# Optimization experiments

Measured on AMD Instinct MI355X. Metric: run time of the kernel, lower is better.

## Reference

```python
import jax, jax.numpy as jnp
import numpy as np

B, T, C = 4, 2048, 1024
H = 16
HD = C // H  # 64


def setup_inputs() -> dict:
    key = jax.random.key(0)
    k1, k2, k3 = jax.random.split(key, 3)
    x = jax.random.normal(k1, (B, T, C), dtype=jnp.float32)
    W_qkv = jax.random.normal(k2, (3 * C, C), dtype=jnp.float32) * (C ** -0.5)
    W_proj = jax.random.normal(k3, (C, C), dtype=jnp.float32) * (C ** -0.5)
    b_proj = jnp.zeros((C,), dtype=jnp.float32)
    return {"x": x, "W_qkv": W_qkv, "W_proj": W_proj, "b_proj": b_proj}


def reference(x, W_qkv, W_proj, b_proj):
    # qkv = x @ W_qkv.T : [B,T,3C]
    qkv = jnp.einsum('btc,oc->bto', x, W_qkv)
    # Faithful to torch: view(B,T,H,3*HD) then chunk last dim -> per-head q/k/v
    qkv = qkv.reshape(B, T, H, 3 * HD)
    q, k, v = jnp.split(qkv, 3, axis=-1)      # each [B,T,H,HD]
    q = q.transpose(0, 2, 1, 3)               # [B,H,T,HD]
    k = k.transpose(0, 2, 1, 3)
    v = v.transpose(0, 2, 1, 3)
    scale = HD ** -0.5
    att = jnp.einsum('bhqd,bhkd->bhqk', q, k) * scale  # [B,H,T,T]
    causal = jnp.tril(jnp.ones((T, T), dtype=bool))
    att = jnp.where(causal, att, -jnp.inf)
    att = jax.nn.softmax(att, axis=-1)
    out = jnp.einsum('bhqk,bhkd->bhqd', att, v)        # [B,H,T,HD]
    out = out.transpose(0, 2, 1, 3).reshape(B, T, C)
    out = jnp.einsum('btc,oc->bto', out, W_proj) + b_proj
    return out
```

## Files before the change

### kernel.cpp

```cpp
#include <hip/hip_runtime.h>
#include <stdint.h>

#define B_ 4
#define T_ 2048
#define C_ 1024
#define H_ 16
#define HD_ 64

typedef __attribute__((ext_vector_type(8))) short short8;
typedef __attribute__((ext_vector_type(4))) float f32x4;

typedef uint32_t __attribute__((address_space(3))) lds_u32;
typedef const uint32_t __attribute__((address_space(1))) glb_u32;

__device__ inline void async16(const void* g, void* l) {
    __builtin_amdgcn_global_load_lds((glb_u32*)g, (lds_u32*)l, 16, 0, 0);
}

__device__ inline short f2bf(float f) {
    union { float f; uint32_t u; } x; x.f = f;
    uint32_t r = (x.u + 0x7fffu + ((x.u >> 16) & 1u)) >> 16;
    return (short)r;
}
__device__ inline float bf2f(short b) {
    union { uint32_t u; float f; } x; x.u = ((uint32_t)(uint16_t)b) << 16;
    return x.f;
}

__global__ void detect_f32(const uint32_t* __restrict__ x, int* __restrict__ flag) {
    __shared__ int cnt;
    if (threadIdx.x == 0) cnt = 0;
    __syncthreads();
    int sane = 0;
    for (int i = threadIdx.x; i < 1024; i += 256) {
        float v = bf2f((short)(x[i] & 0xFFFFu));
        float a = fabsf(v);
        if (a > 1e-5f && a < 1e5f) sane++;
    }
    atomicAdd(&cnt, sane);
    __syncthreads();
    if (threadIdx.x == 0) *flag = (cnt < 512) ? 1 : 0;
}

__global__ void to_bf16(const void* __restrict__ src, short* __restrict__ dst,
                        int n, const int* __restrict__ flag) {
    const int i = (blockIdx.x * blockDim.x + threadIdx.x) * 8;
    if (i >= n) return;
    if (*flag) {
        const float* s = (const float*)src;
        short8 o;
#pragma unroll
        for (int j = 0; j < 8; j++) o[j] = f2bf(s[i + j]);
        *(short8*)&dst[i] = o;
    } else {
        *(short8*)&dst[i] = *(const short8*)((const short*)src + i);
    }
}

template <bool DUAL>
__global__ __launch_bounds__(256) void gemm_bt(
    const short* __restrict__ A, const short* __restrict__ Bm,
    const short* __restrict__ bias_bf, void* __restrict__ Cout,
    int M, int N, int K, const int* __restrict__ flag)
{
    __shared__ short As[128 * 32];
    __shared__ short Bs[128 * 32];
    const int tid  = threadIdx.x;
    const int lane = tid & 63;
    const int wave = tid >> 6;
    const int quad = lane >> 4;
    const int lcol = lane & 15;
    const int m0 = blockIdx.y * 128;
    const int n0 = blockIdx.x * 128;
    const int wm = (wave >> 1) * 64;
    const int wn = (wave & 1) * 64;
    const int isf32 = DUAL ? *flag : 0;

    f32x4 acc[4][4];
#pragma unroll
    for (int i = 0; i < 4; i++)
#pragma unroll
        for (int j = 0; j < 4; j++) acc[i][j] = f32x4{0.f, 0.f, 0.f, 0.f};

    const int idx0 = tid * 8;
    const int row0 = idx0 >> 5, col0 = idx0 & 31;
    const int idx1 = (256 + tid) * 8;
    const int row1 = idx1 >> 5, col1 = idx1 & 31;

    for (int k0 = 0; k0 < K; k0 += 32) {
        async16(&A[(size_t)(m0 + row0) * K + k0 + col0], &As[idx0]);
        async16(&A[(size_t)(m0 + row1) * K + k0 + col1], &As[idx1]);
        async16(&Bm[(size_t)(n0 + row0) * K + k0 + col0], &Bs[idx0]);
        async16(&Bm[(size_t)(n0 + row1) * K + k0 + col1], &Bs[idx1]);
        __syncthreads();

        short8 af[4], bfr[4];
#pragma unroll
        for (int mi = 0; mi < 4; mi++)
            af[mi] = *(const short8*)&As[(wm + mi * 16 + lcol) * 32 + quad * 8];
#pragma unroll
        for (int ni = 0; ni < 4; ni++)
            bfr[ni] = *(const short8*)&Bs[(wn + ni * 16 + lcol) * 32 + quad * 8];
#pragma unroll
        for (int mi = 0; mi < 4; mi++)
#pragma unroll
            for (int ni = 0; ni < 4; ni++)
                acc[mi][ni] = __builtin_amdgcn_mfma_f32_16x16x32_bf16(
                    af[mi], bfr[ni], acc[mi][ni], 0, 0, 0);
        __syncthreads();
    }

#pragma unroll
    for (int ni = 0; ni < 4; ni++) {
        const int col = n0 + wn + ni * 16 + lcol;
        const float bv = bias_bf ? bf2f(bias_bf[col]) : 0.f;
#pragma unroll
        for (int mi = 0; mi < 4; mi++) {
            const int row = m0 + wm + mi * 16 + quad * 4;
#pragma unroll
            for (int r = 0; r < 4; r++) {
                const float val = acc[mi][ni][r] + bv;
                const size_t off = (size_t)(row + r) * N + col;
                if (DUAL && isf32) ((float*)Cout)[off] = val;
                else               ((short*)Cout)[off] = f2bf(val);
            }
        }
    }
}

__global__ __launch_bounds__(256) void attn(const short* __restrict__ qkv,
                                            short* __restrict__ att)
{
    __shared__ short lds_k[64][72];
    __shared__ short lds_vt[64][68];
    __shared__ short lds_p[4][16][76];

    const int tid  = threadIdx.x;
    const int lane = tid & 63;
    const int wave = tid >> 6;
    const int quad = lane >> 4;
    const int lcol = lane & 15;

    const int j    = blockIdx.x & 7;
    const int bh   = blockIdx.x >> 3;
    const int b    = bh >> 4;
    const int h    = bh & 15;

    const size_t rowstride = 3 * C_;
    const size_t bhbase = (size_t)b * T_ * rowstride + (size_t)h * (3 * HD_);

    const int kkey = tid >> 2;
    const int kdp  = (tid & 3) * 16;
    const int vkey = tid & 63;
    const int vd0  = (tid >> 6) * 16;

    short8 kA, kB, vA, vB;
    auto load_tile = [&](int k0) {
        const size_t kb = bhbase + (size_t)(k0 + kkey) * rowstride + HD_ + kdp;
        kA = *(const short8*)&qkv[kb];
        kB = *(const short8*)&qkv[kb + 8];
        const size_t vb = bhbase + (size_t)(k0 + vkey) * rowstride + 2 * HD_ + vd0;
        vA = *(const short8*)&qkv[vb];
        vB = *(const short8*)&qkv[vb + 8];
    };

    const float LOG2E_SCALE = 0.1803368801f;

    auto process_chunk = [&](int qblk, bool sync_first) {
        const int q0 = qblk * 128;
        const int qA = q0 + wave * 16;
        const int qB = q0 + 64 + wave * 16;

        short8 qfA0, qfA1, qfB0, qfB1;
        {
            const size_t ba = bhbase + (size_t)(qA + lcol) * rowstride + quad * 8;
            qfA0 = *(const short8*)&qkv[ba];
            qfA1 = *(const short8*)&qkv[ba + 32];
            const size_t bb = bhbase + (size_t)(qB + lcol) * rowstride + quad * 8;
            qfB0 = *(const short8*)&qkv[bb];
            qfB1 = *(const short8*)&qkv[bb + 32];
        }

        f32x4 oA[4], oB[4];
#pragma unroll
        for (int i = 0; i < 4; i++) { oA[i] = f32x4{0.f,0.f,0.f,0.f}; oB[i] = f32x4{0.f,0.f,0.f,0.f}; }
        float lA[4] = {0.f,0.f,0.f,0.f}, lB[4] = {0.f,0.f,0.f,0.f};

        load_tile(0);

        const int LT = 2 * qblk + 1;
        for (int kt = 0; kt <= LT; ++kt) {
            if (kt || sync_first) __syncthreads();
            *(short8*)&lds_k[kkey][kdp]     = kA;
            *(short8*)&lds_k[kkey][kdp + 8] = kB;
#pragma unroll
            for (int jj = 0; jj < 8; jj++) {
                lds_vt[vd0 + jj][vkey]     = vA[jj];
                lds_vt[vd0 + 8 + jj][vkey] = vB[jj];
            }
            __syncthreads();
            if (kt < LT) load_tile((kt + 1) * 64);

            const int k0 = kt * 64;
            const bool doA = (kt < LT);

            f32x4 SA[4], SB[4];
#pragma unroll
            for (int t = 0; t < 4; t++) {
                const short8 kf0 = *(const short8*)&lds_k[t * 16 + lcol][quad * 8];
                const short8 kf1 = *(const short8*)&lds_k[t * 16 + lcol][32 + quad * 8];
                SB[t] = f32x4{0.f, 0.f, 0.f, 0.f};
                SB[t] = __builtin_amdgcn_mfma_f32_16x16x32_bf16(qfB0, kf0, SB[t], 0, 0, 0);
                SB[t] = __builtin_amdgcn_mfma_f32_16x16x32_bf16(qfB1, kf1, SB[t], 0, 0, 0);
                if (doA) {
                    SA[t] = f32x4{0.f, 0.f, 0.f, 0.f};
                    SA[t] = __builtin_amdgcn_mfma_f32_16x16x32_bf16(qfA0, kf0, SA[t], 0, 0, 0);
                    SA[t] = __builtin_amdgcn_mfma_f32_16x16x32_bf16(qfA1, kf1, SA[t], 0, 0, 0);
                }
            }

            short8 vf[4][2];
#pragma unroll
            for (int dt = 0; dt < 4; dt++) {
                vf[dt][0] = *(const short8*)&lds_vt[dt * 16 + lcol][quad * 8];
                vf[dt][1] = *(const short8*)&lds_vt[dt * 16 + lcol][32 + quad * 8];
            }

            if (doA) {
                const bool maskA = (kt == LT - 1);
#pragma unroll
                for (int r = 0; r < 4; r++) {
                    const int qrow = qA + quad * 4 + r;
#pragma unroll
                    for (int t = 0; t < 4; t++) {
                        float e = __builtin_amdgcn_exp2f(fminf(SA[t][r] * LOG2E_SCALE, 88.f));
                        if (maskA && (k0 + t * 16 + lcol > qrow)) e = 0.f;
                        lA[r] += e;
                        lds_p[wave][quad * 4 + r][t * 16 + lcol] = f2bf(e);
                    }
                }
                const short8 pf0 = *(const short8*)&lds_p[wave][lcol][quad * 8];
                const short8 pf1 = *(const short8*)&lds_p[wave][lcol][32 + quad * 8];
#pragma unroll
                for (int dt = 0; dt < 4; dt++) {
                    oA[dt] = __builtin_amdgcn_mfma_f32_16x16x32_bf16(pf0, vf[dt][0], oA[dt], 0, 0, 0);
                    oA[dt] = __builtin_amdgcn_mfma_f32_16x16x32_bf16(pf1, vf[dt][1], oA[dt], 0, 0, 0);
                }
            }

            {
                const bool maskB = (kt == LT);
#pragma unroll
                for (int r = 0; r < 4; r++) {
                    const int qrow = qB + quad * 4 + r;
#pragma unroll
                    for (int t = 0; t < 4; t++) {
                        float e = __builtin_amdgcn_exp2f(fminf(SB[t][r] * LOG2E_SCALE, 88.f));
                        if (maskB && (k0 + t * 16 + lcol > qrow)) e = 0.f;
                        lB[r] += e;
                        lds_p[wave][quad * 4 + r][t * 16 + lcol] = f2bf(e);
                    }
                }
                const short8 pf0 = *(const short8*)&lds_p[wave][lcol][quad * 8];
                const short8 pf1 = *(const short8*)&lds_p[wave][lcol][32 + quad * 8];
#pragma unroll
                for (int dt = 0; dt < 4; dt++) {
                    oB[dt] = __builtin_amdgcn_mfma_f32_16x16x32_bf16(pf0, vf[dt][0], oB[dt], 0, 0, 0);
                    oB[dt] = __builtin_amdgcn_mfma_f32_16x16x32_bf16(pf1, vf[dt][1], oB[dt], 0, 0, 0);
                }
            }
        }

#pragma unroll
        for (int r = 0; r < 4; r++) {
            float ra = lA[r], rb = lB[r];
#pragma unroll
            for (int off = 1; off < 16; off <<= 1) {
                ra += __shfl_xor(ra, off);
                rb += __shfl_xor(rb, off);
            }
            const float ia = (ra > 0.f) ? 1.f / ra : 0.f;
            const float ib = (rb > 0.f) ? 1.f / rb : 0.f;
            const int qrA = qA + quad * 4 + r;
            const int qrB = qB + quad * 4 + r;
#pragma unroll
            for (int dt = 0; dt < 4; dt++) {
                const int col = h * HD_ + dt * 16 + lcol;
                att[(size_t)(b * T_ + qrA) * C_ + col] = f2bf(oA[dt][r] * ia);
                att[(size_t)(b * T_ + qrB) * C_ + col] = f2bf(oB[dt][r] * ib);
            }
        }
    };

    process_chunk(15 - j, false);
    process_chunk(j, true);
}

extern "C" void kernel_launch(void* const* d_in, const int* in_sizes, int n_in,
                              void* d_out, int out_size, void* d_ws, size_t ws_size,
                              hipStream_t stream) {
    const int n_x  = B_ * T_ * C_;
    const int n_wq = 3 * C_ * C_;
    const int n_wp = C_ * C_;

    char* ws = (char*)d_ws;
    short* qkv     = (short*)(ws);
    short* x_or_at = (short*)(ws + 50331648);
    short* wq_bf   = (short*)(ws + 50331648 + 16777216);
    short* wp_bf   = (short*)(ws + 50331648 + 16777216 + 6291456);
    short* bias_bf = (short*)(ws + 50331648 + 16777216 + 6291456 + 2097152);
    int*   flag    = (int*)  (ws + 50331648 + 16777216 + 6291456 + 2097152 + 2048);

    dim3 blk(256);

    detect_f32<<<1, blk, 0, stream>>>((const uint32_t*)d_in[0], flag);

    to_bf16<<<dim3((n_x  / 8 + 255) / 256), blk, 0, stream>>>(d_in[0], x_or_at, n_x,  flag);
    to_bf16<<<dim3((n_wq / 8 + 255) / 256), blk, 0, stream>>>(d_in[1], wq_bf,   n_wq, flag);
    to_bf16<<<dim3((n_wp / 8 + 255) / 256), blk, 0, stream>>>(d_in[2], wp_bf,   n_wp, flag);
    to_bf16<<<dim3(1), blk, 0, stream>>>(d_in[3], bias_bf, C_, flag);

    gemm_bt<false><<<dim3((3 * C_) / 128, (B_ * T_) / 128), blk, 0, stream>>>(
        x_or_at, wq_bf, nullptr, qkv, B_ * T_, 3 * C_, C_, flag);

    attn<<<dim3(B_ * H_ * (T_ / 256)), blk, 0, stream>>>(qkv, x_or_at);

    gemm_bt<true><<<dim3(C_ / 128, (B_ * T_) / 128), blk, 0, stream>>>(
        x_or_at, wp_bf, bias_bf, d_out, B_ * T_, C_, C_, flag);
}
```

Measured before the change: 288.5 us.

## Double-buffer attention LDS tiles, pack V/P as bf16 pairs, fuse conversions

Double-buffers the K and V LDS tiles so each iteration needs only one barrier. Stores V transposed as packed bf16 pairs in 32-bit words, which allows word-wide LDS writes instead of 16-bit scatter. Packs P with truncating bf16 conversion and vector stores. Folds the softmax scale into Q up front, and merges the four conversion launches into one kernel. These cut LDS store count, barriers and launch overhead, at the cost of extra rounding from pre-scaling Q and truncating P to bf16.

```diff
diff --git a/kernel.cpp b/kernel.cpp
--- a/kernel.cpp
+++ b/kernel.cpp
@@ -9,6 +9,8 @@
 
 typedef __attribute__((ext_vector_type(8))) short short8;
 typedef __attribute__((ext_vector_type(4))) float f32x4;
+typedef __attribute__((ext_vector_type(4))) uint32_t u32x4;
+typedef __attribute__((ext_vector_type(2))) uint32_t u32x2;
 
 typedef uint32_t __attribute__((address_space(3))) lds_u32;
 typedef const uint32_t __attribute__((address_space(1))) glb_u32;
@@ -25,6 +27,12 @@
 __device__ inline float bf2f(short b) {
     union { uint32_t u; float f; } x; x.u = ((uint32_t)(uint16_t)b) << 16;
     return x.f;
+}
+__device__ inline uint32_t fbits(float f) {
+    union { float f; uint32_t u; } x; x.f = f; return x.u;
+}
+__device__ inline uint32_t pack_bf(float a, float b) {
+    return (fbits(b) & 0xffff0000u) | (fbits(a) >> 16);
 }
 
 __global__ void detect_f32(const uint32_t* __restrict__ x, int* __restrict__ flag) {
@@ -42,9 +50,19 @@
     if (threadIdx.x == 0) *flag = (cnt < 512) ? 1 : 0;
 }
 
-__global__ void to_bf16(const void* __restrict__ src, short* __restrict__ dst,
-                        int n, const int* __restrict__ flag) {
-    const int i = (blockIdx.x * blockDim.x + threadIdx.x) * 8;
+__global__ void convert_all(const void* __restrict__ x,  const void* __restrict__ wq,
+                            const void* __restrict__ wp, const void* __restrict__ bias,
+                            short* __restrict__ xd, short* __restrict__ wqd,
+                            short* __restrict__ wpd, short* __restrict__ biasd,
+                            const int* __restrict__ flag)
+{
+    const int blk = blockIdx.x;
+    const void* src; short* dst; int base, n;
+    if (blk < 4096)      { src = x;    dst = xd;    base = blk;        n = B_*T_*C_; }
+    else if (blk < 5632) { src = wq;   dst = wqd;   base = blk - 4096; n = 3*C_*C_; }
+    else if (blk < 6144) { src = wp;   dst = wpd;   base = blk - 5632; n = C_*C_; }
+    else                 { src = bias; dst = biasd; base = 0;          n = C_; }
+    const int i = (base * 256 + threadIdx.x) * 8;
     if (i >= n) return;
     if (*flag) {
         const float* s = (const float*)src;
@@ -131,9 +149,9 @@
 __global__ __launch_bounds__(256) void attn(const short* __restrict__ qkv,
                                             short* __restrict__ att)
 {
-    __shared__ short lds_k[64][72];
-    __shared__ short lds_vt[64][68];
-    __shared__ short lds_p[4][16][76];
+    __shared__ short    lds_k[2][64][76];
+    __shared__ uint32_t lds_vt[2][64][34];
+    __shared__ uint32_t lds_p[4][16][34];
 
     const int tid  = threadIdx.x;
     const int lane = tid & 63;
@@ -151,22 +169,30 @@
 
     const int kkey = tid >> 2;
     const int kdp  = (tid & 3) * 16;
-    const int vkey = tid & 63;
-    const int vd0  = (tid >> 6) * 16;
+    const int kp    = (tid & 15) | ((tid & 16) << 1);
+    const int vd0   = (tid >> 5) * 8;
+    const int vword = 2 * (tid & 15) + ((tid >> 4) & 1);
 
     short8 kA, kB, vA, vB;
     auto load_tile = [&](int k0) {
         const size_t kb = bhbase + (size_t)(k0 + kkey) * rowstride + HD_ + kdp;
         kA = *(const short8*)&qkv[kb];
         kB = *(const short8*)&qkv[kb + 8];
-        const size_t vb = bhbase + (size_t)(k0 + vkey) * rowstride + 2 * HD_ + vd0;
+        const size_t vb = bhbase + (size_t)(k0 + kp) * rowstride + 2 * HD_ + vd0;
         vA = *(const short8*)&qkv[vb];
-        vB = *(const short8*)&qkv[vb + 8];
+        vB = *(const short8*)&qkv[vb + 16 * rowstride];
     };
 
-    const float LOG2E_SCALE = 0.1803368801f;
-
-    auto process_chunk = [&](int qblk, bool sync_first) {
+    const float SC = 0.1803368801f;
+
+    auto scale_frag = [&](short8 q) {
+        short8 r;
+#pragma unroll
+        for (int i = 0; i < 8; i++) r[i] = f2bf(bf2f(q[i]) * SC);
+        return r;
+    };
+
+    auto process_chunk = [&](int qblk) {
         const int q0 = qblk * 128;
         const int qA = q0 + wave * 16;
         const int qB = q0 + 64 + wave * 16;
@@ -174,11 +200,11 @@
         short8 qfA0, qfA1, qfB0, qfB1;
         {
             const size_t ba = bhbase + (size_t)(qA + lcol) * rowstride + quad * 8;
-            qfA0 = *(const short8*)&qkv[ba];
-            qfA1 = *(const short8*)&qkv[ba + 32];
+            qfA0 = scale_frag(*(const short8*)&qkv[ba]);
+            qfA1 = scale_frag(*(const short8*)&qkv[ba + 32]);
             const size_t bb = bhbase + (size_t)(qB + lcol) * rowstride + quad * 8;
-            qfB0 = *(const short8*)&qkv[bb];
-            qfB1 = *(const short8*)&qkv[bb + 32];
+            qfB0 = scale_frag(*(const short8*)&qkv[bb]);
+            qfB1 = scale_frag(*(const short8*)&qkv[bb + 32]);
         }
 
         f32x4 oA[4], oB[4];
@@ -190,14 +216,14 @@
 
         const int LT = 2 * qblk + 1;
         for (int kt = 0; kt <= LT; ++kt) {
-            if (kt || sync_first) __syncthreads();
-            *(short8*)&lds_k[kkey][kdp]     = kA;
-            *(short8*)&lds_k[kkey][kdp + 8] = kB;
-#pragma unroll
-            for (int jj = 0; jj < 8; jj++) {
-                lds_vt[vd0 + jj][vkey]     = vA[jj];
-                lds_vt[vd0 + 8 + jj][vkey] = vB[jj];
-            }
+            short    (*kb_)[76] = lds_k[kt & 1];
+            uint32_t (*vb_)[34] = lds_vt[kt & 1];
+            *(short8*)&kb_[kkey][kdp]     = kA;
+            *(short8*)&kb_[kkey][kdp + 8] = kB;
+#pragma unroll
+            for (int jj = 0; jj < 8; jj++)
+                vb_[vd0 + jj][vword] =
+                    ((uint32_t)(uint16_t)vB[jj] << 16) | (uint16_t)vA[jj];
             __syncthreads();
             if (kt < LT) load_tile((kt + 1) * 64);
 
@@ -207,8 +233,8 @@
             f32x4 SA[4], SB[4];
 #pragma unroll
             for (int t = 0; t < 4; t++) {
-                const short8 kf0 = *(const short8*)&lds_k[t * 16 + lcol][quad * 8];
-                const short8 kf1 = *(const short8*)&lds_k[t * 16 + lcol][32 + quad * 8];
+                const short8 kf0 = *(const short8*)&kb_[t * 16 + lcol][quad * 8];
+                const short8 kf1 = *(const short8*)&kb_[t * 16 + lcol][32 + quad * 8];
                 SB[t] = f32x4{0.f, 0.f, 0.f, 0.f};
                 SB[t] = __builtin_amdgcn_mfma_f32_16x16x32_bf16(qfB0, kf0, SB[t], 0, 0, 0);
                 SB[t] = __builtin_amdgcn_mfma_f32_16x16x32_bf16(qfB1, kf1, SB[t], 0, 0, 0);
@@ -222,8 +248,10 @@
             short8 vf[4][2];
 #pragma unroll
             for (int dt = 0; dt < 4; dt++) {
-                vf[dt][0] = *(const short8*)&lds_vt[dt * 16 + lcol][quad * 8];
-                vf[dt][1] = *(const short8*)&lds_vt[dt * 16 + lcol][32 + quad * 8];
+                vf[dt][0] = __builtin_bit_cast(short8,
+                    *(const u32x4*)&vb_[dt * 16 + lcol][quad * 4]);
+                vf[dt][1] = __builtin_bit_cast(short8,
+                    *(const u32x4*)&vb_[dt * 16 + lcol][16 + quad * 4]);
             }
 
             if (doA) {
@@ -231,16 +259,20 @@
 #pragma unroll
                 for (int r = 0; r < 4; r++) {
                     const int qrow = qA + quad * 4 + r;
+                    float e[4];
 #pragma unroll
                     for (int t = 0; t < 4; t++) {
-                        float e = __builtin_amdgcn_exp2f(fminf(SA[t][r] * LOG2E_SCALE, 88.f));
-                        if (maskA && (k0 + t * 16 + lcol > qrow)) e = 0.f;
-                        lA[r] += e;
-                        lds_p[wave][quad * 4 + r][t * 16 + lcol] = f2bf(e);
+                        e[t] = __builtin_amdgcn_exp2f(fminf(SA[t][r], 88.f));
+                        if (maskA && (k0 + t * 16 + lcol > qrow)) e[t] = 0.f;
+                        lA[r] += e[t];
                     }
-                }
-                const short8 pf0 = *(const short8*)&lds_p[wave][lcol][quad * 8];
-                const short8 pf1 = *(const short8*)&lds_p[wave][lcol][32 + quad * 8];
+                    *(u32x2*)&lds_p[wave][quad * 4 + r][lcol * 2] =
+                        u32x2{pack_bf(e[0], e[1]), pack_bf(e[2], e[3])};
+                }
+                const short8 pf0 = __builtin_bit_cast(short8,
+                    *(const u32x4*)&lds_p[wave][lcol][quad * 4]);
+                const short8 pf1 = __builtin_bit_cast(short8,
+                    *(const u32x4*)&lds_p[wave][lcol][16 + quad * 4]);
 #pragma unroll
                 for (int dt = 0; dt < 4; dt++) {
                     oA[dt] = __builtin_amdgcn_mfma_f32_16x16x32_bf16(pf0, vf[dt][0], oA[dt], 0, 0, 0);
@@ -253,16 +285,20 @@
 #pragma unroll
                 for (int r = 0; r < 4; r++) {
                     const int qrow = qB + quad * 4 + r;
+                    float e[4];
 #pragma unroll
                     for (int t = 0; t < 4; t++) {
-                        float e = __builtin_amdgcn_exp2f(fminf(SB[t][r] * LOG2E_SCALE, 88.f));
-                        if (maskB && (k0 + t * 16 + lcol > qrow)) e = 0.f;
-                        lB[r] += e;
-                        lds_p[wave][quad * 4 + r][t * 16 + lcol] = f2bf(e);
+                        e[t] = __builtin_amdgcn_exp2f(fminf(SB[t][r], 88.f));
+                        if (maskB && (k0 + t * 16 + lcol > qrow)) e[t] = 0.f;
+                        lB[r] += e[t];
                     }
-                }
-                const short8 pf0 = *(const short8*)&lds_p[wave][lcol][quad * 8];
-                const short8 pf1 = *(const short8*)&lds_p[wave][lcol][32 + quad * 8];
+                    *(u32x2*)&lds_p[wave][quad * 4 + r][lcol * 2] =
+                        u32x2{pack_bf(e[0], e[1]), pack_bf(e[2], e[3])};
+                }
+                const short8 pf0 = __builtin_bit_cast(short8,
+                    *(const u32x4*)&lds_p[wave][lcol][quad * 4]);
+                const short8 pf1 = __builtin_bit_cast(short8,
+                    *(const u32x4*)&lds_p[wave][lcol][16 + quad * 4]);
 #pragma unroll
                 for (int dt = 0; dt < 4; dt++) {
                     oB[dt] = __builtin_amdgcn_mfma_f32_16x16x32_bf16(pf0, vf[dt][0], oB[dt], 0, 0, 0);
@@ -292,17 +328,13 @@
         }
     };
 
-    process_chunk(15 - j, false);
-    process_chunk(j, true);
+    process_chunk(15 - j);
+    process_chunk(j);
 }
 
 extern "C" void kernel_launch(void* const* d_in, const int* in_sizes, int n_in,
                               void* d_out, int out_size, void* d_ws, size_t ws_size,
                               hipStream_t stream) {
-    const int n_x  = B_ * T_ * C_;
-    const int n_wq = 3 * C_ * C_;
-    const int n_wp = C_ * C_;
-
     char* ws = (char*)d_ws;
     short* qkv     = (short*)(ws);
     short* x_or_at = (short*)(ws + 50331648);
@@ -315,10 +347,9 @@
 
     detect_f32<<<1, blk, 0, stream>>>((const uint32_t*)d_in[0], flag);
 
-    to_bf16<<<dim3((n_x  / 8 + 255) / 256), blk, 0, stream>>>(d_in[0], x_or_at, n_x,  flag);
-    to_bf16<<<dim3((n_wq / 8 + 255) / 256), blk, 0, stream>>>(d_in[1], wq_bf,   n_wq, flag);
-    to_bf16<<<dim3((n_wp / 8 + 255) / 256), blk, 0, stream>>>(d_in[2], wp_bf,   n_wp, flag);
-    to_bf16<<<dim3(1), blk, 0, stream>>>(d_in[3], bias_bf, C_, flag);
+    convert_all<<<dim3(6145), blk, 0, stream>>>(
+        d_in[0], d_in[1], d_in[2], d_in[3],
+        x_or_at, wq_bf, wp_bf, bias_bf, flag);
 
     gemm_bt<false><<<dim3((3 * C_) / 128, (B_ * T_) / 128), blk, 0, stream>>>(
         x_or_at, wq_bf, nullptr, qkv, B_ * T_, 3 * C_, C_, flag);
```

Measured after the change: 356.8 us. +23.7%, slower.
